# Optimization experiments

Measured on AMD Instinct MI355X. Metric: run time of the kernel, lower is better.

Reference implementation:

```python
import jax, jax.numpy as jnp
import numpy as np

EMBED_DIM = 1024
NUM_HEADS = 16
HEAD_DIM = EMBED_DIM // NUM_HEADS
ROPE_BASE = 10000.0
NEG_INF = -1e9


def _rope_tables(T, dim, dtype=jnp.float32):
    inv_freq = 1.0 / (ROPE_BASE ** (jnp.arange(0, dim, 2, dtype=jnp.float32) / dim))
    t = jnp.arange(T, dtype=jnp.float32)
    freqs = jnp.einsum('t,f->tf', t, inv_freq)          # [T, dim/2]
    emb = jnp.concatenate([freqs, freqs], axis=-1)       # [T, dim]
    return jnp.cos(emb).astype(dtype), jnp.sin(emb).astype(dtype)


def _rotate_half(x):
    x1, x2 = jnp.split(x, 2, axis=-1)
    return jnp.concatenate([-x2, x1], axis=-1)


def setup_inputs() -> dict:
    key = jax.random.key(0)
    kx, kqkv, kout = jax.random.split(key, 3)
    B, T = 2, 2048
    x = jax.random.normal(kx, (B, T, EMBED_DIM), dtype=jnp.float32)
    # Dense kernels (no bias), glorot-ish scale
    w_qkv = jax.random.normal(kqkv, (EMBED_DIM, 3 * EMBED_DIM), dtype=jnp.float32) * (EMBED_DIM ** -0.5)
    w_out = jax.random.normal(kout, (EMBED_DIM, EMBED_DIM), dtype=jnp.float32) * (EMBED_DIM ** -0.5)
    return {"x": x, "w_qkv": w_qkv, "w_out": w_out}


def reference(x, w_qkv, w_out):
    B, T, _ = x.shape
    qkv = x @ w_qkv                                      # [B, T, 3E]
    q, k, v = jnp.split(qkv, 3, axis=-1)

    def split_heads(t):
        return t.reshape(B, T, NUM_HEADS, HEAD_DIM).transpose(0, 2, 1, 3)  # [B,H,T,D]

    q, k, v = split_heads(q), split_heads(k), split_heads(v)

    cos, sin = _rope_tables(T, HEAD_DIM, x.dtype)        # [T, D]
    cos = cos[None, None, :, :]
    sin = sin[None, None, :, :]
    q = q * cos + _rotate_half(q) * sin
    k = k * cos + _rotate_half(k) * sin

    scale = jnp.sqrt(jnp.asarray(HEAD_DIM, dtype=jnp.float32)).astype(x.dtype)
    scores = jnp.einsum('bhqd,bhkd->bhqk', q, k) / scale  # [B,H,T,T]
    causal = jnp.tril(jnp.ones((T, T), dtype=bool))[None, None, :, :]
    scores = jnp.where(causal, scores, jnp.asarray(NEG_INF, dtype=x.dtype))
    probs = jax.nn.softmax(scores, axis=-1)
    out = jnp.einsum('bhqk,bhkd->bhqd', probs, v)         # [B,H,T,D]
    out = out.transpose(0, 2, 1, 3).reshape(B, T, EMBED_DIM)
    return out @ w_out
```

## Files before the change

kernel.cpp:

```cpp
#include <hip/hip_runtime.h>
#include <hip/hip_bf16.h>
#include <cstdint>

#define DI __device__ __forceinline__

using u16x8  = __attribute__((ext_vector_type(8))) unsigned short;
using u32x4  = __attribute__((ext_vector_type(4))) unsigned int;
using bf16x8 = __attribute__((ext_vector_type(8))) __bf16;
using f32x4  = __attribute__((ext_vector_type(4))) float;


DI unsigned short f2bf(float f) {
  unsigned u = __builtin_bit_cast(unsigned, f);
  u += 0x7fffu + ((u >> 16) & 1u);
  return (unsigned short)(u >> 16);
}
DI float bf2f(unsigned short b) {
  unsigned u = (unsigned)b << 16;
  return __builtin_bit_cast(float, u);
}
DI unsigned cvt_pk_bf16(float lo, float hi) {
  unsigned r;
  asm("v_cvt_pk_bf16_f32 %0, %1, %2" : "=v"(r) : "v"(lo), "v"(hi));
  return r;
}
DI void permlane_swap32(unsigned& a, unsigned& b) {
  asm("v_permlane32_swap_b32 %0, %1" : "+v"(a), "+v"(b));
}
DI void permlane_swap16(unsigned& a, unsigned& b) {
  asm("v_permlane16_swap_b32 %0, %1" : "+v"(a), "+v"(b));
}

DI void gld_lds16(const void* g, void* l) {
  __builtin_amdgcn_global_load_lds(
      (const __attribute__((address_space(1))) void*)(uintptr_t)g,
      (__attribute__((address_space(3))) void*)(uint32_t)(uintptr_t)l,
      16, 0, 0);
}


__global__ __launch_bounds__(256) void cvt_bf16_kernel(const float* __restrict__ in,
                                                        unsigned short* __restrict__ out, int n) {
  int i = (blockIdx.x * 256 + threadIdx.x) * 8;
  if (i >= n) return;
  float4 v0 = *(const float4*)(in + i);
  float4 v1 = *(const float4*)(in + i + 4);
  u16x8 o;
  o[0] = f2bf(v0.x); o[1] = f2bf(v0.y); o[2] = f2bf(v0.z); o[3] = f2bf(v0.w);
  o[4] = f2bf(v1.x); o[5] = f2bf(v1.y); o[6] = f2bf(v1.z); o[7] = f2bf(v1.w);
  *(u16x8*)(out + i) = o;
}

__global__ __launch_bounds__(256) void transpose_cvt_kernel(const float* __restrict__ in,
                                                             unsigned short* __restrict__ out,
                                                             int K, int N) {
  __shared__ float tile[32][33];
  int n0 = blockIdx.x * 32, k0 = blockIdx.y * 32;
  int tx = threadIdx.x & 31, ty = threadIdx.x >> 5;
#pragma unroll
  for (int i = 0; i < 4; ++i)
    tile[ty * 4 + i][tx] = in[(size_t)(k0 + ty * 4 + i) * N + n0 + tx];
  __syncthreads();
#pragma unroll
  for (int i = 0; i < 4; ++i)
    out[(size_t)(n0 + ty * 4 + i) * K + k0 + tx] = f2bf(tile[tx][ty * 4 + i]);
}


template <int MT>
DI void rope_rows(const f32x4 (&acc)[8][4], unsigned short* __restrict__ dst,
                  int gm0, int h, float qs, int r15, int g4) {
#pragma unroll
  for (int r = 0; r < 4; ++r) {
    int mrow = gm0 + MT * 16 + g4 * 4 + r;
    int b = mrow >> 11, t = mrow & 2047;
    unsigned short* rowp = dst + (((size_t)(b * 16 + h) * 2048 + t) << 6);
    float tf = (float)t;
#pragma unroll
    for (int nt = 0; nt < 2; ++nt) {
      int j = nt * 16 + r15;
      float invf = exp2f((float)j * -0.4152410118609203f);
      float ang = tf * invf;
      float sv, cv;
      sincosf(ang, &sv, &cv);
      float x1 = acc[MT][nt][r], x2 = acc[MT][nt + 2][r];
      rowp[j]      = f2bf((x1 * cv - x2 * sv) * qs);
      rowp[j + 32] = f2bf((x2 * cv + x1 * sv) * qs);
    }
  }
}

template <int P>
DI void vtrans_pass(const f32x4 (&acc)[8][4], short* __restrict__ tb,
                    unsigned short* __restrict__ vhead, int t0, int lane, int r15, int g4) {
#pragma unroll
  for (int np = 0; np < 2; ++np)
#pragma unroll
    for (int mt = 0; mt < 8; ++mt)
#pragma unroll
      for (int pr = 0; pr < 2; ++pr) {
        unsigned pk = cvt_pk_bf16(acc[mt][2 * P + np][2 * pr], acc[mt][2 * P + np][2 * pr + 1]);
        *(unsigned*)(tb + (np * 16 + r15) * 136 + mt * 16 + g4 * 4 + pr * 2) = pk;
      }
#pragma unroll
  for (int cc = 0; cc < 8; ++cc) {
    int dl = (cc & 3) * 8 + (lane >> 3);
    int tc = (lane & 7) * 8 + (cc >> 2) * 64;
    u16x8 vv = *(const u16x8*)(tb + dl * 136 + tc);
    *(u16x8*)(vhead + (size_t)(P * 32 + dl) * 2048 + t0 + tc) = vv;
  }
}


__global__ __launch_bounds__(512, 2)
void gemm256_qkv(const unsigned short* __restrict__ A, const unsigned short* __restrict__ B,
                 unsigned short* __restrict__ q_out, unsigned short* __restrict__ k_out,
                 unsigned short* __restrict__ v_out, int M, int N, int K) {
  __shared__ __align__(16) char smem[2][65536];
  const int tid = threadIdx.x;
  const int lane = tid & 63, wave = tid >> 6;
  const int wr = wave >> 2, wc = wave & 3;
  const int r15 = lane & 15, g4 = lane >> 4;

  const int id = blockIdx.x;
  const int g = (id & 7) * 24 + (id >> 3);
  const int by = g / 12, bx = g % 12;
  const int m0 = by << 8, n0 = bx << 8;

  const size_t Ks = (size_t)K;
  const unsigned short* aptr = A + (size_t)(m0 + wave * 32 + r15) * Ks + g4 * 8;
  const unsigned short* bptr = B + (size_t)(n0 + wave * 32 + r15) * Ks + g4 * 8;

  f32x4 acc[8][4] = {};
  const int NT = K >> 6;

  auto stage = [&](int buf, int kt) {
    const unsigned short* ak = aptr + kt * 64;
    const unsigned short* bk = bptr + kt * 64;
    char* sA = &smem[buf][0]     + wave * 4096;
    char* sB = &smem[buf][32768] + wave * 4096;
    gld_lds16(ak,                sA);
    gld_lds16(ak + 32,           sA + 1024);
    gld_lds16(ak + 16 * Ks,      sA + 2048);
    gld_lds16(ak + 16 * Ks + 32, sA + 3072);
    gld_lds16(bk,                sB);
    gld_lds16(bk + 32,           sB + 1024);
    gld_lds16(bk + 16 * Ks,      sB + 2048);
    gld_lds16(bk + 16 * Ks + 32, sB + 3072);
  };

  stage(0, 0);
  __syncthreads();
  for (int kt = 0; kt < NT; ++kt) {
    const int buf = kt & 1;
    if (kt + 1 < NT) stage(buf ^ 1, kt + 1);
    const char* baseA = &smem[buf][0];
    const char* baseB = &smem[buf][32768];
#pragma unroll
    for (int kc = 0; kc < 2; ++kc) {
      bf16x8 af[8], bfr[4];
#pragma unroll
      for (int mt = 0; mt < 8; ++mt)
        af[mt] = *(const bf16x8*)(baseA + (((wr * 8 + mt) * 2 + kc) << 10) + lane * 16);
#pragma unroll
      for (int nt = 0; nt < 4; ++nt)
        bfr[nt] = *(const bf16x8*)(baseB + (((wc * 4 + nt) * 2 + kc) << 10) + lane * 16);
      __builtin_amdgcn_s_setprio(1);
#pragma unroll
      for (int mt = 0; mt < 8; ++mt)
#pragma unroll
        for (int nt = 0; nt < 4; ++nt)
          acc[mt][nt] = __builtin_amdgcn_mfma_f32_16x16x32_bf16(af[mt], bfr[nt], acc[mt][nt], 0, 0, 0);
      __builtin_amdgcn_s_setprio(0);
    }
    __syncthreads();
  }

  const int gm0 = m0 + wr * 128, gn0 = n0 + wc * 64;
  const int region = gn0 >> 10;
  const int h = (gn0 & 1023) >> 6;
  if (region <= 1) {
    unsigned short* dst = (region == 0) ? q_out : k_out;
    const float qs = (region == 0) ? (0.125f * 1.44269504088896341f) : 1.0f;
    rope_rows<0>(acc, dst, gm0, h, qs, r15, g4);
    rope_rows<1>(acc, dst, gm0, h, qs, r15, g4);
    rope_rows<2>(acc, dst, gm0, h, qs, r15, g4);
    rope_rows<3>(acc, dst, gm0, h, qs, r15, g4);
    rope_rows<4>(acc, dst, gm0, h, qs, r15, g4);
    rope_rows<5>(acc, dst, gm0, h, qs, r15, g4);
    rope_rows<6>(acc, dst, gm0, h, qs, r15, g4);
    rope_rows<7>(acc, dst, gm0, h, qs, r15, g4);
  } else {
    const int b = gm0 >> 11, t0 = gm0 & 2047;
    unsigned short* vhead = v_out + ((size_t)(b * 16 + h) * 64) * 2048;
    short* tb = (short*)(&smem[0][0] + wave * 16384);
    vtrans_pass<0>(acc, tb, vhead, t0, lane, r15, g4);
    vtrans_pass<1>(acc, tb, vhead, t0, lane, r15, g4);
  }
}


__global__ __launch_bounds__(256)
void gemm_proj(const unsigned short* __restrict__ A, const unsigned short* __restrict__ B,
               float* __restrict__ c_out, int M, int N, int K) {
  __shared__ __align__(16) char smem[2][16384];
  const int tid = threadIdx.x;
  const int lane = tid & 63, wave = tid >> 6;
  const int wm = wave >> 1, wn = wave & 1;

  const int id = blockIdx.x;
  const int xcd = id & 7, rr = id >> 3;
  const int bx = xcd, by = rr;
  const int m0 = by << 7, n0 = bx << 7;

  const int r15 = lane & 15, g4 = lane >> 4;

  const size_t Ks = (size_t)K;
  const unsigned short* aptr = A + (size_t)(m0 + wave * 16 + r15) * Ks + g4 * 8;
  const unsigned short* bptr = B + (size_t)(n0 + wave * 16 + r15) * Ks + g4 * 8;

  f32x4 acc[4][4] = {};
  const int NT = K >> 5;

  auto stage = [&](int buf, int kt) {
    const unsigned short* ak = aptr + kt * 32;
    const unsigned short* bk = bptr + kt * 32;
    char* sA = &smem[buf][0] + wave * 1024;
    char* sB = &smem[buf][8192] + wave * 1024;
    gld_lds16(ak, sA);
    gld_lds16(ak + 64 * Ks, sA + 4096);
    gld_lds16(bk, sB);
    gld_lds16(bk + 64 * Ks, sB + 4096);
  };

  stage(0, 0);
  __syncthreads();
  for (int kt = 0; kt < NT; ++kt) {
    int buf = kt & 1;
    if (kt + 1 < NT) stage(buf ^ 1, kt + 1);
    const char* base = &smem[buf][0];
    bf16x8 af[4], bfr[4];
#pragma unroll
    for (int mt = 0; mt < 4; ++mt)
      af[mt] = *(const bf16x8*)(base + ((wm * 4 + mt) * 64 + lane) * 16);
#pragma unroll
    for (int nt = 0; nt < 4; ++nt)
      bfr[nt] = *(const bf16x8*)(base + 8192 + ((wn * 4 + nt) * 64 + lane) * 16);
#pragma unroll
    for (int mt = 0; mt < 4; ++mt)
#pragma unroll
      for (int nt = 0; nt < 4; ++nt)
        acc[mt][nt] = __builtin_amdgcn_mfma_f32_16x16x32_bf16(af[mt], bfr[nt], acc[mt][nt], 0, 0, 0);
    __syncthreads();
  }

  const int gm0 = m0 + wm * 64, gn0 = n0 + wn * 64;
#pragma unroll
  for (int mt = 0; mt < 4; ++mt)
#pragma unroll
    for (int r = 0; r < 4; ++r) {
      int mrow = gm0 + mt * 16 + g4 * 4 + r;
      float* rowp = c_out + (size_t)mrow * N + gn0;
#pragma unroll
      for (int nt = 0; nt < 4; ++nt)
        rowp[nt * 16 + r15] = acc[mt][nt][r];
    }
}


__device__ const int RBMAP[24] = {7, 23, 20, 21, 18, 19, 17, 5,
                                  22, 6, 16, 12, 13, 14, 15, 10,
                                  0, 1, 2, 3, 8, 9, 4, 11};

__global__ __launch_bounds__(256)
void attn_fused(const unsigned short* __restrict__ qb, const unsigned short* __restrict__ kb,
                const unsigned short* __restrict__ vt, unsigned short* __restrict__ attno,
                unsigned short* __restrict__ pO, float* __restrict__ pml) {
  __shared__ __align__(16) char ksm[2][8192];
  __shared__ __align__(16) char vsm[2][8192];

  const int tid = threadIdx.x, lane = tid & 63, wave = tid >> 6;
  const int r15 = lane & 15, g4 = lane >> 4;

  const int wg = blockIdx.x;
  const int qq = wg >> 3;
  const int bh = (wg & 7) * 4 + qq / 24;
  const int rb = RBMAP[qq % 24];
  int J, c; bool multi;
  if (rb < 8) { J = rb; c = 0; multi = false; }
  else { int rr = rb - 8; J = 8 + (rr >> 1); c = rr & 1; multi = true; }
  const int ntw = 2 * J + 2;
  const int ktmid = J + 1;
  const int kt0 = (multi && c) ? ktmid : 0;
  const int ktN = multi ? (c ? ntw : ktmid) : ntw;
  const int q0 = J << 7;
  const int q0w = q0 + wave * 32;

  const size_t hb = (size_t)bh * 2048 * 64;
  const unsigned short* Qp = qb + hb;
  const unsigned short* Kp = kb + hb;
  const unsigned short* Vp = vt + hb;

  bf16x8 qf[2][2];
#pragma unroll
  for (int mq = 0; mq < 2; ++mq)
#pragma unroll
    for (int kc = 0; kc < 2; ++kc)
      qf[mq][kc] = *(const bf16x8*)(Qp + (size_t)(q0w + mq * 16 + r15) * 64 + kc * 32 + g4 * 8);

  f32x4 o[2][4] = {};
  float mr[2] = {-INFINITY, -INFINITY};
  float lr[2] = {0.f, 0.f};

  auto stage = [&](int buf, int kt) {
    const int kv0 = kt << 6;
#pragma unroll
    for (int i = 0; i < 2; ++i) {
      int f = wave * 2 + i;
      int nt = f >> 1, kc = f & 1;
      gld_lds16(Kp + (size_t)(kv0 + nt * 16 + r15) * 64 + kc * 32 + g4 * 8, &ksm[buf][f * 1024]);
      gld_lds16(Vp + (size_t)(nt * 16 + r15) * 2048 + kv0 + kc * 32 + g4 * 8, &vsm[buf][f * 1024]);
    }
  };

  auto process = [&](int buf, int kv0, bool mask) {
    bf16x8 kf[8];
#pragma unroll
    for (int i = 0; i < 8; ++i)
      kf[i] = *(const bf16x8*)(&ksm[buf][i * 1024] + lane * 16);

    f32x4 s[4][2] = {};
    __builtin_amdgcn_s_setprio(1);
#pragma unroll
    for (int nt = 0; nt < 4; ++nt)
#pragma unroll
      for (int kc = 0; kc < 2; ++kc) {
        s[nt][0] = __builtin_amdgcn_mfma_f32_16x16x32_bf16(kf[nt * 2 + kc], qf[0][kc], s[nt][0], 0, 0, 0);
        s[nt][1] = __builtin_amdgcn_mfma_f32_16x16x32_bf16(kf[nt * 2 + kc], qf[1][kc], s[nt][1], 0, 0, 0);
      }
    __builtin_amdgcn_s_setprio(0);

    if (mask) {
#pragma unroll
      for (int nt = 0; nt < 4; ++nt)
#pragma unroll
        for (int mq = 0; mq < 2; ++mq)
#pragma unroll
          for (int r = 0; r < 4; ++r)
            if (kv0 + nt * 16 + g4 * 4 + r > q0w + mq * 16 + r15) s[nt][mq][r] = -1e9f;
    }

    bf16x8 pa[2][2];
#pragma unroll
    for (int mq = 0; mq < 2; ++mq) {
      float m0 = fmaxf(fmaxf(s[0][mq][0], s[0][mq][1]), fmaxf(s[0][mq][2], s[0][mq][3]));
      float m1 = fmaxf(fmaxf(s[1][mq][0], s[1][mq][1]), fmaxf(s[1][mq][2], s[1][mq][3]));
      float m2 = fmaxf(fmaxf(s[2][mq][0], s[2][mq][1]), fmaxf(s[2][mq][2], s[2][mq][3]));
      float m3 = fmaxf(fmaxf(s[3][mq][0], s[3][mq][1]), fmaxf(s[3][mq][2], s[3][mq][3]));
      float mx = fmaxf(fmaxf(m0, m1), fmaxf(m2, m3));
      mx = fmaxf(mx, __shfl_xor(mx, 16));
      mx = fmaxf(mx, __shfl_xor(mx, 32));
      float mnew;
      if (!__all(mx <= mr[mq] + 8.f)) {
        mnew = fmaxf(mr[mq], mx);
        float fsc = exp2f(mr[mq] - mnew);
        mr[mq] = mnew;
        lr[mq] *= fsc;
#pragma unroll
        for (int r = 0; r < 4; ++r) {
          float fr = __shfl(fsc, (g4 << 2) + r);
#pragma unroll
          for (int dt = 0; dt < 4; ++dt) o[mq][dt][r] *= fr;
        }
      } else {
        mnew = mr[mq];
      }
      float t0 = 0.f, t1 = 0.f, t2 = 0.f, t3 = 0.f;
#pragma unroll
      for (int nt = 0; nt < 4; ++nt) {
        float p0 = exp2f(s[nt][mq][0] - mnew);
        float p1 = exp2f(s[nt][mq][1] - mnew);
        float p2 = exp2f(s[nt][mq][2] - mnew);
        float p3 = exp2f(s[nt][mq][3] - mnew);
        s[nt][mq][0] = p0; s[nt][mq][1] = p1; s[nt][mq][2] = p2; s[nt][mq][3] = p3;
        if (nt == 0) t0 = (p0 + p1) + (p2 + p3);
        if (nt == 1) t1 = (p0 + p1) + (p2 + p3);
        if (nt == 2) t2 = (p0 + p1) + (p2 + p3);
        if (nt == 3) t3 = (p0 + p1) + (p2 + p3);
      }
      float ps = (t0 + t1) + (t2 + t3);
      ps += __shfl_xor(ps, 16);
      ps += __shfl_xor(ps, 32);
      lr[mq] += ps;
      unsigned p32[4][2];
#pragma unroll
      for (int nt = 0; nt < 4; ++nt) {
        p32[nt][0] = cvt_pk_bf16(s[nt][mq][0], s[nt][mq][1]);
        p32[nt][1] = cvt_pk_bf16(s[nt][mq][2], s[nt][mq][3]);
      }
#pragma unroll
      for (int kc = 0; kc < 2; ++kc) {
        u32x4 w;
#pragma unroll
        for (int pi = 0; pi < 2; ++pi) {
          unsigned a = p32[2 * kc][pi], b = p32[2 * kc + 1][pi];
          permlane_swap32(a, b);
          permlane_swap16(a, b);
          w[pi] = a;
          w[2 + pi] = b;
        }
        pa[mq][kc] = __builtin_bit_cast(bf16x8, w);
      }
    }

    bf16x8 vf[8];
#pragma unroll
    for (int i = 0; i < 8; ++i)
      vf[i] = *(const bf16x8*)(&vsm[buf][i * 1024] + lane * 16);

    __builtin_amdgcn_s_setprio(1);
#pragma unroll
    for (int kc = 0; kc < 2; ++kc)
#pragma unroll
      for (int dt = 0; dt < 4; ++dt) {
        o[0][dt] = __builtin_amdgcn_mfma_f32_16x16x32_bf16(pa[0][kc], vf[dt * 2 + kc], o[0][dt], 0, 0, 0);
        o[1][dt] = __builtin_amdgcn_mfma_f32_16x16x32_bf16(pa[1][kc], vf[dt * 2 + kc], o[1][dt], 0, 0, 0);
      }
    __builtin_amdgcn_s_setprio(0);
  };

  int buf = 0;
  stage(0, kt0);
  __syncthreads();
  for (int kt = kt0; kt < ktN; ++kt) {
    if (kt + 1 < ktN) stage(buf ^ 1, kt + 1);
    const int kv0 = kt << 6;
    if (kv0 <= q0w + 31)
      process(buf, kv0, kv0 + 63 > q0w);
    __syncthreads();
    buf ^= 1;
  }

  if (!multi) {
    const int b = bh >> 4, h = bh & 15;
#pragma unroll
    for (int mq = 0; mq < 2; ++mq) {
      float inv = 1.f / lr[mq];
#pragma unroll
      for (int r = 0; r < 4; ++r) {
        float ir = __shfl(inv, (g4 << 2) + r);
        int q = q0w + mq * 16 + g4 * 4 + r;
        unsigned short* rowp = attno + (size_t)(b * 2048 + q) * 1024 + h * 64;
#pragma unroll
        for (int dt = 0; dt < 4; ++dt)
          rowp[dt * 16 + r15] = f2bf(o[mq][dt][r] * ir);
      }
    }
  } else {
    const int sidx = (bh * 8 + (J - 8)) * 2 + c;
    unsigned short* po = pO + (size_t)sidx * 8192 + wave * 32 * 64;
#pragma unroll
    for (int mq = 0; mq < 2; ++mq)
#pragma unroll
      for (int r = 0; r < 4; ++r)
#pragma unroll
        for (int dt = 0; dt < 4; ++dt)
          po[(mq * 16 + g4 * 4 + r) * 64 + dt * 16 + r15] = f2bf(o[mq][dt][r]);
    if (g4 == 0) {
      float* pm = pml + sidx * 256 + wave * 32;
#pragma unroll
      for (int mq = 0; mq < 2; ++mq) {
        pm[mq * 16 + r15] = mr[mq];
        pm[128 + mq * 16 + r15] = lr[mq];
      }
    }
  }
}

__global__ __launch_bounds__(256)
void attn_combine(const unsigned short* __restrict__ pO, const float* __restrict__ pml,
                  unsigned short* __restrict__ attno) {
  const int bx = blockIdx.x;
  const int bh = bx >> 3, Jrel = bx & 7, J = 8 + Jrel;
  const int t = threadIdx.x;
  const int row = t >> 1;
  const int dh = (t & 1) << 5;
  const int s0i = (bh * 8 + Jrel) * 2;
  const float* pm0 = pml + s0i * 256;
  const float* pm1 = pm0 + 256;
  float m0 = pm0[row], l0 = pm0[128 + row];
  float m1 = pm1[row], l1 = pm1[128 + row];
  float mg = fmaxf(m0, m1);
  float s0 = exp2f(m0 - mg), s1 = exp2f(m1 - mg);
  float inv = 1.f / (l0 * s0 + l1 * s1);
  s0 *= inv; s1 *= inv;
  const unsigned short* o0 = pO + (size_t)s0i * 8192 + row * 64 + dh;
  const unsigned short* o1 = o0 + 8192;
  const int b = bh >> 4, h = bh & 15;
  const int q = J * 128 + row;
  unsigned short* dst = attno + (size_t)(b * 2048 + q) * 1024 + h * 64 + dh;
#pragma unroll
  for (int dd = 0; dd < 32; dd += 8) {
    u16x8 a = *(const u16x8*)(o0 + dd);
    u16x8 bq = *(const u16x8*)(o1 + dd);
    u16x8 ov;
#pragma unroll
    for (int e = 0; e < 8; ++e)
      ov[e] = f2bf(bf2f(a[e]) * s0 + bf2f(bq[e]) * s1);
    *(u16x8*)(dst + dd) = ov;
  }
}


extern "C" void kernel_launch(void* const* d_in, const int* in_sizes, int n_in,
                              void* d_out, int out_size, void* d_ws, size_t ws_size,
                              hipStream_t stream) {
  const float* x     = (const float*)d_in[0];
  const float* w_qkv = (const float*)d_in[1];
  const float* w_out = (const float*)d_in[2];
  float* out = (float*)d_out;

  char* ws = (char*)d_ws;
  unsigned short* xb  = (unsigned short*)(ws);
  unsigned short* wqT = (unsigned short*)(ws + (8u << 20));
  unsigned short* woT = (unsigned short*)(ws + (14u << 20));
  unsigned short* qb  = (unsigned short*)(ws + (16u << 20));
  unsigned short* kb  = (unsigned short*)(ws + (24u << 20));
  unsigned short* vt  = (unsigned short*)(ws + (32u << 20));
  unsigned short* ao  = (unsigned short*)(ws + (40u << 20));
  unsigned short* pO  = xb;
  float*          pml = (float*)wqT;

  cvt_bf16_kernel<<<2048, 256, 0, stream>>>(x, xb, 4096 * 1024);
  transpose_cvt_kernel<<<dim3(96, 32), 256, 0, stream>>>(w_qkv, wqT, 1024, 3072);
  transpose_cvt_kernel<<<dim3(32, 32), 256, 0, stream>>>(w_out, woT, 1024, 1024);
  gemm256_qkv<<<192, 512, 0, stream>>>(xb, wqT, qb, kb, vt, 4096, 3072, 1024);
  attn_fused<<<768, 256, 0, stream>>>(qb, kb, vt, ao, pO, pml);
  attn_combine<<<256, 256, 0, stream>>>(pO, pml, ao);
  gemm_proj<<<256, 256, 0, stream>>>(ao, woT, out, 4096, 1024, 1024);
}
```

Before: 153.8 us.

## Deepen QKV and projection GEMM pipelines to four-slot LDS ring with vmcnt waits

Both the QKV GEMM and the output projection GEMM move from double-buffered 64/32-wide K tiles with a full __syncthreads per step to a 4-slot ring of 32-wide K tiles. Loads for tile t+3 are issued after the current fragments are read, and explicit s_waitcnt vmcnt plus a bare s_barrier replace the full sync. The aim is to keep more global loads in flight and hide memory latency behind MFMA work. In exchange there are twice as many barriers per K in QKV, the hand-counted vmcnt values can be fragile, and occupancy hints change for the projection kernel.

Result: faster. 143.6 us (-6.7%).

```diff
diff --git a/kernel.cpp b/kernel.cpp
--- a/kernel.cpp
+++ b/kernel.cpp
@@ -37,6 +37,11 @@
       (__attribute__((address_space(3))) void*)(uint32_t)(uintptr_t)l,
       16, 0, 0);
 }
+
+DI void wait_vm8() { asm volatile("s_waitcnt vmcnt(8)" ::: "memory"); }
+DI void wait_vm4() { asm volatile("s_waitcnt vmcnt(4)" ::: "memory"); }
+DI void wait_vm0() { asm volatile("s_waitcnt vmcnt(0)" ::: "memory"); }
+DI void sched_fence() { asm volatile("" ::: "memory"); }
 
 
 __global__ __launch_bounds__(256) void cvt_bf16_kernel(const float* __restrict__ in,
@@ -116,7 +121,7 @@
 void gemm256_qkv(const unsigned short* __restrict__ A, const unsigned short* __restrict__ B,
                  unsigned short* __restrict__ q_out, unsigned short* __restrict__ k_out,
                  unsigned short* __restrict__ v_out, int M, int N, int K) {
-  __shared__ __align__(16) char smem[2][65536];
+  __shared__ __align__(16) char smem[4][32768];
   const int tid = threadIdx.x;
   const int lane = tid & 63, wave = tid >> 6;
   const int wr = wave >> 2, wc = wave & 3;
@@ -132,49 +137,54 @@
   const unsigned short* bptr = B + (size_t)(n0 + wave * 32 + r15) * Ks + g4 * 8;
 
   f32x4 acc[8][4] = {};
-  const int NT = K >> 6;
-
-  auto stage = [&](int buf, int kt) {
-    const unsigned short* ak = aptr + kt * 64;
-    const unsigned short* bk = bptr + kt * 64;
-    char* sA = &smem[buf][0]     + wave * 4096;
-    char* sB = &smem[buf][32768] + wave * 4096;
-    gld_lds16(ak,                sA);
-    gld_lds16(ak + 32,           sA + 1024);
-    gld_lds16(ak + 16 * Ks,      sA + 2048);
-    gld_lds16(ak + 16 * Ks + 32, sA + 3072);
-    gld_lds16(bk,                sB);
-    gld_lds16(bk + 32,           sB + 1024);
-    gld_lds16(bk + 16 * Ks,      sB + 2048);
-    gld_lds16(bk + 16 * Ks + 32, sB + 3072);
+  const int NT = K >> 5;
+
+  auto stage = [&](int slot, int tt) {
+    const unsigned short* ak = aptr + tt * 32;
+    const unsigned short* bk = bptr + tt * 32;
+    char* sA = &smem[slot][0]     + wave * 2048;
+    char* sB = &smem[slot][16384] + wave * 2048;
+    gld_lds16(ak,           sA);
+    gld_lds16(ak + 16 * Ks, sA + 1024);
+    gld_lds16(bk,           sB);
+    gld_lds16(bk + 16 * Ks, sB + 1024);
   };
 
-  stage(0, 0);
+  auto body = [&](int t) {
+    sched_fence();
+    const char* sA = &smem[t & 3][0];
+    const char* sB = &smem[t & 3][16384];
+    bf16x8 af[8], bfr[4];
+#pragma unroll
+    for (int mt = 0; mt < 8; ++mt)
+      af[mt] = *(const bf16x8*)(sA + (wr * 8 + mt) * 1024 + lane * 16);
+#pragma unroll
+    for (int nt = 0; nt < 4; ++nt)
+      bfr[nt] = *(const bf16x8*)(sB + (wc * 4 + nt) * 1024 + lane * 16);
+    if (t + 3 < NT) stage((t + 3) & 3, t + 3);
+    __builtin_amdgcn_s_setprio(1);
+#pragma unroll
+    for (int mt = 0; mt < 8; ++mt)
+#pragma unroll
+      for (int nt = 0; nt < 4; ++nt)
+        acc[mt][nt] = __builtin_amdgcn_mfma_f32_16x16x32_bf16(af[mt], bfr[nt], acc[mt][nt], 0, 0, 0);
+    __builtin_amdgcn_s_setprio(0);
+  };
+
+  stage(0, 0); stage(1, 1); stage(2, 2);
+  for (int t = 0; t < NT - 2; ++t) {
+    wait_vm8();
+    __builtin_amdgcn_s_barrier();
+    body(t);
+  }
+  wait_vm4();
+  __builtin_amdgcn_s_barrier();
+  body(NT - 2);
+  wait_vm0();
+  __builtin_amdgcn_s_barrier();
+  body(NT - 1);
+
   __syncthreads();
-  for (int kt = 0; kt < NT; ++kt) {
-    const int buf = kt & 1;
-    if (kt + 1 < NT) stage(buf ^ 1, kt + 1);
-    const char* baseA = &smem[buf][0];
-    const char* baseB = &smem[buf][32768];
-#pragma unroll
-    for (int kc = 0; kc < 2; ++kc) {
-      bf16x8 af[8], bfr[4];
-#pragma unroll
-      for (int mt = 0; mt < 8; ++mt)
-        af[mt] = *(const bf16x8*)(baseA + (((wr * 8 + mt) * 2 + kc) << 10) + lane * 16);
-#pragma unroll
-      for (int nt = 0; nt < 4; ++nt)
-        bfr[nt] = *(const bf16x8*)(baseB + (((wc * 4 + nt) * 2 + kc) << 10) + lane * 16);
-      __builtin_amdgcn_s_setprio(1);
-#pragma unroll
-      for (int mt = 0; mt < 8; ++mt)
-#pragma unroll
-        for (int nt = 0; nt < 4; ++nt)
-          acc[mt][nt] = __builtin_amdgcn_mfma_f32_16x16x32_bf16(af[mt], bfr[nt], acc[mt][nt], 0, 0, 0);
-      __builtin_amdgcn_s_setprio(0);
-    }
-    __syncthreads();
-  }
 
   const int gm0 = m0 + wr * 128, gn0 = n0 + wc * 64;
   const int region = gn0 >> 10;
@@ -200,59 +210,70 @@
 }
 
 
-__global__ __launch_bounds__(256)
+__global__ __launch_bounds__(256, 2)
 void gemm_proj(const unsigned short* __restrict__ A, const unsigned short* __restrict__ B,
                float* __restrict__ c_out, int M, int N, int K) {
-  __shared__ __align__(16) char smem[2][16384];
+  __shared__ __align__(16) char smem[4][16384];
   const int tid = threadIdx.x;
   const int lane = tid & 63, wave = tid >> 6;
   const int wm = wave >> 1, wn = wave & 1;
+  const int r15 = lane & 15, g4 = lane >> 4;
 
   const int id = blockIdx.x;
   const int xcd = id & 7, rr = id >> 3;
-  const int bx = xcd, by = rr;
-  const int m0 = by << 7, n0 = bx << 7;
-
-  const int r15 = lane & 15, g4 = lane >> 4;
+  const int m0 = rr << 7, n0 = xcd << 7;
 
   const size_t Ks = (size_t)K;
-  const unsigned short* aptr = A + (size_t)(m0 + wave * 16 + r15) * Ks + g4 * 8;
-  const unsigned short* bptr = B + (size_t)(n0 + wave * 16 + r15) * Ks + g4 * 8;
+  const unsigned short* aptr = A + (size_t)(m0 + wave * 32 + r15) * Ks + g4 * 8;
+  const unsigned short* bptr = B + (size_t)(n0 + wave * 32 + r15) * Ks + g4 * 8;
 
   f32x4 acc[4][4] = {};
   const int NT = K >> 5;
 
-  auto stage = [&](int buf, int kt) {
-    const unsigned short* ak = aptr + kt * 32;
-    const unsigned short* bk = bptr + kt * 32;
-    char* sA = &smem[buf][0] + wave * 1024;
-    char* sB = &smem[buf][8192] + wave * 1024;
-    gld_lds16(ak, sA);
-    gld_lds16(ak + 64 * Ks, sA + 4096);
-    gld_lds16(bk, sB);
-    gld_lds16(bk + 64 * Ks, sB + 4096);
+  auto stage = [&](int slot, int tt) {
+    const unsigned short* ak = aptr + tt * 32;
+    const unsigned short* bk = bptr + tt * 32;
+    char* sA = &smem[slot][0]    + wave * 2048;
+    char* sB = &smem[slot][8192] + wave * 2048;
+    gld_lds16(ak,           sA);
+    gld_lds16(ak + 16 * Ks, sA + 1024);
+    gld_lds16(bk,           sB);
+    gld_lds16(bk + 16 * Ks, sB + 1024);
   };
 
-  stage(0, 0);
-  __syncthreads();
-  for (int kt = 0; kt < NT; ++kt) {
-    int buf = kt & 1;
-    if (kt + 1 < NT) stage(buf ^ 1, kt + 1);
-    const char* base = &smem[buf][0];
+  auto body = [&](int t) {
+    sched_fence();
+    const char* sA = &smem[t & 3][0];
+    const char* sB = &smem[t & 3][8192];
     bf16x8 af[4], bfr[4];
 #pragma unroll
     for (int mt = 0; mt < 4; ++mt)
-      af[mt] = *(const bf16x8*)(base + ((wm * 4 + mt) * 64 + lane) * 16);
+      af[mt] = *(const bf16x8*)(sA + (wm * 4 + mt) * 1024 + lane * 16);
 #pragma unroll
     for (int nt = 0; nt < 4; ++nt)
-      bfr[nt] = *(const bf16x8*)(base + 8192 + ((wn * 4 + nt) * 64 + lane) * 16);
+      bfr[nt] = *(const bf16x8*)(sB + (wn * 4 + nt) * 1024 + lane * 16);
+    if (t + 3 < NT) stage((t + 3) & 3, t + 3);
+    __builtin_amdgcn_s_setprio(1);
 #pragma unroll
     for (int mt = 0; mt < 4; ++mt)
 #pragma unroll
       for (int nt = 0; nt < 4; ++nt)
         acc[mt][nt] = __builtin_amdgcn_mfma_f32_16x16x32_bf16(af[mt], bfr[nt], acc[mt][nt], 0, 0, 0);
-    __syncthreads();
-  }
+    __builtin_amdgcn_s_setprio(0);
+  };
+
+  stage(0, 0); stage(1, 1); stage(2, 2);
+  for (int t = 0; t < NT - 2; ++t) {
+    wait_vm8();
+    __builtin_amdgcn_s_barrier();
+    body(t);
+  }
+  wait_vm4();
+  __builtin_amdgcn_s_barrier();
+  body(NT - 2);
+  wait_vm0();
+  __builtin_amdgcn_s_barrier();
+  body(NT - 1);
 
   const int gm0 = m0 + wm * 64, gn0 = n0 + wn * 64;
 #pragma unroll
```
